# Performance work log

Measured on AMD Instinct MI355X. Metric: run time of the kernel, lower is better.

The kernel has to match this reference:

```python
import jax, jax.numpy as jnp
import numpy as np

N_NODES = 100000
N_EDGES = 1600000
NUM_FEATURES = 128
HIDDEN = 64
NUM_CLASSES = 2


def _gcn_norm(edge_index, num_nodes):
    # PyG gcn_norm: add self-loops, symmetric degree normalization.
    loop = jnp.arange(num_nodes, dtype=edge_index.dtype)
    src = jnp.concatenate([edge_index[0], loop])
    dst = jnp.concatenate([edge_index[1], loop])
    deg = jax.ops.segment_sum(jnp.ones_like(src, dtype=jnp.float32), dst,
                              num_segments=num_nodes)
    dinv = jnp.where(deg > 0, jax.lax.rsqrt(deg), 0.0)
    norm = dinv[src] * dinv[dst]  # [E + N]
    return src, dst, norm


def _gcn_conv(x, src, dst, norm, W, b, num_nodes):
    h = x @ W  # linear transform first (PyG GCNConv)
    msg = h[src] * norm[:, None]  # gather + edge scaling, [E+N, H]
    out = jax.ops.segment_sum(msg, dst, num_segments=num_nodes)  # scatter-add
    return out + b


def setup_inputs() -> dict:
    key = jax.random.key(0)
    ks = jax.random.split(key, 8)
    x = jax.random.normal(ks[0], (N_NODES, NUM_FEATURES), dtype=jnp.float32)
    edge_index = jax.random.randint(ks[1], (2, N_EDGES), 0, N_NODES, dtype=jnp.int32)
    def glorot(k, shape):
        lim = np.sqrt(6.0 / (shape[0] + shape[1]))
        return jax.random.uniform(k, shape, jnp.float32, -lim, lim)
    return {
        "x": x,
        "edge_index": edge_index,
        "W1": glorot(ks[2], (NUM_FEATURES, HIDDEN)),
        "b1": jnp.zeros((HIDDEN,), jnp.float32),
        "W2": glorot(ks[3], (HIDDEN, HIDDEN)),
        "b2": jnp.zeros((HIDDEN,), jnp.float32),
        "W3": glorot(ks[4], (HIDDEN, HIDDEN)),
        "b3": jnp.zeros((HIDDEN,), jnp.float32),
        "Wlin": glorot(ks[5], (HIDDEN, NUM_CLASSES)),
        "blin": jnp.zeros((NUM_CLASSES,), jnp.float32),
    }


def reference(x, edge_index, W1, b1, W2, b2, W3, b3, Wlin, blin):
    num_nodes = x.shape[0]
    src, dst, norm = _gcn_norm(edge_index, num_nodes)
    # eval mode: dropout is identity
    h = jax.nn.relu(_gcn_conv(x, src, dst, norm, W1, b1, num_nodes))
    h = jax.nn.relu(_gcn_conv(h, src, dst, norm, W2, b2, num_nodes))
    h = jax.nn.relu(_gcn_conv(h, src, dst, norm, W3, b3, num_nodes))
    logits = h @ Wlin + blin
    return jax.nn.log_softmax(logits, axis=1)
```

## Files before the change

kernel.cpp:

```cpp
#include <hip/hip_runtime.h>
#include <cstdint>
#include <cstddef>

#define NF 128
#define NH 64

typedef unsigned int uint32;

__device__ inline unsigned short f2bf(float f) {
  unsigned int u = __float_as_uint(f);
  return (unsigned short)((u + 0x7FFF + ((u >> 16) & 1)) >> 16);
}
__device__ inline float bf2f_lo(uint32 u) { return __uint_as_float(u << 16); }
__device__ inline float bf2f_hi(uint32 u) { return __uint_as_float(u & 0xFFFF0000u); }


__global__ __launch_bounds__(256) void count_kernel(const int* __restrict__ ei, int E,
                                                    int* __restrict__ cnt, int RW) {
  int pass = blockIdx.x & 7;
  int i = (blockIdx.x >> 3) * 256 + threadIdx.x;
  if (i * 4 >= E) return;
  int4 d = ((const int4*)(ei + E))[i];
  int lo = pass * RW, hi = lo + RW;
  if (d.x >= lo && d.x < hi) atomicAdd(&cnt[d.x], 1);
  if (d.y >= lo && d.y < hi) atomicAdd(&cnt[d.y], 1);
  if (d.z >= lo && d.z < hi) atomicAdd(&cnt[d.z], 1);
  if (d.w >= lo && d.w < hi) atomicAdd(&cnt[d.w], 1);
}

__global__ __launch_bounds__(256) void partial_kernel(const int* __restrict__ cnt, int N,
                                                      int* __restrict__ part) {
  __shared__ int sd[256];
  int t = threadIdx.x;
  int idx = blockIdx.x * 1024 + t * 4;
  int s = 0;
#pragma unroll
  for (int j = 0; j < 4; ++j)
    if (idx + j < N) s += cnt[idx + j];
  sd[t] = s;
  __syncthreads();
  for (int off = 128; off > 0; off >>= 1) {
    if (t < off) sd[t] += sd[t + off];
    __syncthreads();
  }
  if (t == 0) part[blockIdx.x] = sd[0];
}

__global__ __launch_bounds__(128) void scanp_kernel(int* __restrict__ part, int NB,
                                                    int* __restrict__ rowptrN) {
  __shared__ int s[128];
  int t = threadIdx.x;
  int v = (t < NB) ? part[t] : 0;
  s[t] = v;
  __syncthreads();
  for (int off = 1; off < 128; off <<= 1) {
    int add = (t >= off) ? s[t - off] : 0;
    __syncthreads();
    s[t] += add;
    __syncthreads();
  }
  if (t < NB) part[t] = s[t] - v;
  if (t == 0) rowptrN[0] = s[127];
}

__global__ __launch_bounds__(256) void rowptr_kernel(const int* __restrict__ cnt,
                                                     const int* __restrict__ part,
                                                     int* __restrict__ rowptr,
                                                     int* __restrict__ cnt2,
                                                     float* __restrict__ dinv, int N) {
  __shared__ int s[256];
  int t = threadIdx.x;
  int idx = blockIdx.x * 1024 + t * 4;
  int c[4];
  int ts = 0;
#pragma unroll
  for (int j = 0; j < 4; ++j) {
    c[j] = (idx + j < N) ? cnt[idx + j] : 0;
    ts += c[j];
  }
  s[t] = ts;
  __syncthreads();
  for (int off = 1; off < 256; off <<= 1) {
    int add = (t >= off) ? s[t - off] : 0;
    __syncthreads();
    s[t] += add;
    __syncthreads();
  }
  int run = s[t] - ts + part[blockIdx.x];
#pragma unroll
  for (int j = 0; j < 4; ++j) {
    if (idx + j < N) {
      rowptr[idx + j] = run;
      cnt2[idx + j] = run;
      dinv[idx + j] = rsqrtf((float)(c[j] + 1));
    }
    run += c[j];
  }
}

__global__ __launch_bounds__(256) void fill_kernel(const int* __restrict__ ei, int E,
                                                   int* __restrict__ cnt2,
                                                   const float* __restrict__ dinv,
                                                   int2* __restrict__ col2, int RW) {
  int pass = blockIdx.x & 7;
  int i = (blockIdx.x >> 3) * 256 + threadIdx.x;
  if (i * 4 >= E) return;
  int4 sv = ((const int4*)ei)[i];
  int4 dv = ((const int4*)(ei + E))[i];
  int lo = pass * RW, hi = lo + RW;
  int ss[4] = {sv.x, sv.y, sv.z, sv.w};
  int dd[4] = {dv.x, dv.y, dv.z, dv.w};
#pragma unroll
  for (int j = 0; j < 4; ++j) {
    int d = dd[j];
    if (d < lo || d >= hi) continue;
    int s = ss[j];
    float w = dinv[s] * dinv[d];
    int pos = atomicAdd(&cnt2[d], 1);
    col2[pos] = make_int2(s, __float_as_int(w));
  }
}


template <int K>
__global__ __launch_bounds__(256, 4) void gemm_kernel(const float* __restrict__ X,
                                                      const float* __restrict__ W,
                                                      uint32* __restrict__ Hb, int N) {
  __shared__ float XsT[64][68];
  __shared__ float Ws[64 * 64];
  const int tid = threadIdx.x;
  const int n0 = blockIdx.x * 64;
  const int tn = (tid >> 4) * 4;
  const int tf = (tid & 15) * 4;

  float acc[4][4];
#pragma unroll
  for (int i = 0; i < 4; ++i)
#pragma unroll
    for (int j = 0; j < 4; ++j) acc[i][j] = 0.f;

  for (int kt = 0; kt < K / 64; ++kt) {
    {
      const float4* Wg = (const float4*)(W + (size_t)kt * 64 * 64);
      float4* Wl = (float4*)Ws;
#pragma unroll
      for (int j = 0; j < 4; ++j) Wl[tid + j * 256] = Wg[tid + j * 256];
    }
#pragma unroll
    for (int j = 0; j < 4; ++j) {
      int idx = tid + j * 256;
      int n = idx >> 4;
      int kq = idx & 15;
      float4 v = make_float4(0.f, 0.f, 0.f, 0.f);
      if (n0 + n < N)
        v = *(const float4*)(X + (size_t)(n0 + n) * K + kt * 64 + kq * 4);
      XsT[kq * 4 + 0][n] = v.x;
      XsT[kq * 4 + 1][n] = v.y;
      XsT[kq * 4 + 2][n] = v.z;
      XsT[kq * 4 + 3][n] = v.w;
    }
    __syncthreads();
#pragma unroll 8
    for (int k = 0; k < 64; ++k) {
      float4 xv = *(const float4*)(&XsT[k][tn]);
      float4 wv = *(const float4*)(&Ws[k * 64 + tf]);
      acc[0][0] = fmaf(xv.x, wv.x, acc[0][0]);
      acc[0][1] = fmaf(xv.x, wv.y, acc[0][1]);
      acc[0][2] = fmaf(xv.x, wv.z, acc[0][2]);
      acc[0][3] = fmaf(xv.x, wv.w, acc[0][3]);
      acc[1][0] = fmaf(xv.y, wv.x, acc[1][0]);
      acc[1][1] = fmaf(xv.y, wv.y, acc[1][1]);
      acc[1][2] = fmaf(xv.y, wv.z, acc[1][2]);
      acc[1][3] = fmaf(xv.y, wv.w, acc[1][3]);
      acc[2][0] = fmaf(xv.z, wv.x, acc[2][0]);
      acc[2][1] = fmaf(xv.z, wv.y, acc[2][1]);
      acc[2][2] = fmaf(xv.z, wv.z, acc[2][2]);
      acc[2][3] = fmaf(xv.z, wv.w, acc[2][3]);
      acc[3][0] = fmaf(xv.w, wv.x, acc[3][0]);
      acc[3][1] = fmaf(xv.w, wv.y, acc[3][1]);
      acc[3][2] = fmaf(xv.w, wv.z, acc[3][2]);
      acc[3][3] = fmaf(xv.w, wv.w, acc[3][3]);
    }
    __syncthreads();
  }
#pragma unroll
  for (int i = 0; i < 4; ++i) {
    int n = n0 + tn + i;
    if (n < N) {
      uint32 p0 = (uint32)f2bf(acc[i][0]) | ((uint32)f2bf(acc[i][1]) << 16);
      uint32 p1 = (uint32)f2bf(acc[i][2]) | ((uint32)f2bf(acc[i][3]) << 16);
      *(uint2*)(Hb + (size_t)n * 32 + tf / 2) = make_uint2(p0, p1);
    }
  }
}

template <int FINAL>
__global__ __launch_bounds__(256) void prop_fused_kernel(
    const uint32* __restrict__ H32, const int* __restrict__ rowptr,
    const int2* __restrict__ col2, const float* __restrict__ dinv,
    const float* __restrict__ bias, const float* __restrict__ Wn,
    const float* __restrict__ blin, void* __restrict__ outv, int N) {
  __shared__ float Ws[64 * 64];
  __shared__ float rbuf[4][64];
  const int lane = threadIdx.x & 63;
  const int widx = threadIdx.x >> 6;
  const int fl = lane & 31;
  const int half = lane >> 5;

  if (!FINAL) {
    const float4* Wg = (const float4*)Wn;
    float4* Wl = (float4*)Ws;
    for (int i = threadIdx.x; i < 1024; i += 256) Wl[i] = Wg[i];
    __syncthreads();
  }

  int n = blockIdx.x * 4 + widx;
  n = __builtin_amdgcn_readfirstlane(n);
  if (n >= N) return;

  int e0 = rowptr[n];
  int e1 = rowptr[n + 1];
  float di = dinv[n];
  const int2* ec = col2 + e0;
  const int m = e1 - e0;

  float acc0 = 0.f, acc1 = 0.f;
  if (half == 0) {
    uint32 u = H32[(size_t)n * 32 + fl];
    float w = di * di;
    acc0 = bf2f_lo(u) * w;
    acc1 = bf2f_hi(u) * w;
  }

  const int npair = m >> 1;
  const int nfull = npair >> 3;
  for (int b = 0; b < nfull; ++b) {
    int s[8];
    float wv[8];
#pragma unroll
    for (int j = 0; j < 8; ++j) {
      int2 c = ec[2 * (b * 8 + j) + half];
      s[j] = c.x;
      wv[j] = __int_as_float(c.y);
    }
    uint32 u[8];
#pragma unroll
    for (int j = 0; j < 8; ++j) u[j] = H32[(size_t)s[j] * 32 + fl];
#pragma unroll
    for (int j = 0; j < 8; ++j) {
      acc0 = fmaf(wv[j], bf2f_lo(u[j]), acc0);
      acc1 = fmaf(wv[j], bf2f_hi(u[j]), acc1);
    }
  }
  for (int t = nfull * 8; t < npair; ++t) {
    int2 c = ec[2 * t + half];
    uint32 u = H32[(size_t)c.x * 32 + fl];
    float w = __int_as_float(c.y);
    acc0 = fmaf(w, bf2f_lo(u), acc0);
    acc1 = fmaf(w, bf2f_hi(u), acc1);
  }
  if ((m & 1) && half == 0) {
    int2 c = ec[m - 1];
    uint32 u = H32[(size_t)c.x * 32 + fl];
    float w = __int_as_float(c.y);
    acc0 = fmaf(w, bf2f_lo(u), acc0);
    acc1 = fmaf(w, bf2f_hi(u), acc1);
  }
  acc0 += __shfl_xor(acc0, 32, 64);
  acc1 += __shfl_xor(acc1, 32, 64);

  float2 bv = ((const float2*)bias)[fl];
  float r0 = acc0 + bv.x;
  float r1 = acc1 + bv.y;
  r0 = r0 > 0.f ? r0 : 0.f;
  r1 = r1 > 0.f ? r1 : 0.f;

  if (FINAL) {
    float t0 = 0.f, t1 = 0.f;
    if (half == 0) {
      t0 = r0 * Wn[4 * fl + 0] + r1 * Wn[4 * fl + 2];
      t1 = r0 * Wn[4 * fl + 1] + r1 * Wn[4 * fl + 3];
    }
#pragma unroll
    for (int off = 32; off > 0; off >>= 1) {
      t0 += __shfl_xor(t0, off, 64);
      t1 += __shfl_xor(t1, off, 64);
    }
    if (lane == 0) {
      float* out = (float*)outv;
      float l0 = t0 + blin[0];
      float l1 = t1 + blin[1];
      float mx = fmaxf(l0, l1);
      float lz = mx + logf(expf(l0 - mx) + expf(l1 - mx));
      out[(size_t)n * 2 + 0] = l0 - lz;
      out[(size_t)n * 2 + 1] = l1 - lz;
    }
  } else {
    if (half == 0) *(float2*)(&rbuf[widx][2 * fl]) = make_float2(r0, r1);
    __builtin_amdgcn_wave_barrier();
    float o = 0.f;
#pragma unroll
    for (int q = 0; q < 16; ++q) {
      float4 rv = *(const float4*)(&rbuf[widx][4 * q]);
      o = fmaf(rv.x, Ws[(4 * q + 0) * 64 + lane], o);
      o = fmaf(rv.y, Ws[(4 * q + 1) * 64 + lane], o);
      o = fmaf(rv.z, Ws[(4 * q + 2) * 64 + lane], o);
      o = fmaf(rv.w, Ws[(4 * q + 3) * 64 + lane], o);
    }
    ((unsigned short*)outv)[(size_t)n * 64 + lane] = f2bf(o);
  }
}


extern "C" void kernel_launch(void* const* d_in, const int* in_sizes, int n_in,
                              void* d_out, int out_size, void* d_ws, size_t ws_size,
                              hipStream_t stream) {
  const float* x  = (const float*)d_in[0];
  const int*   ei = (const int*)d_in[1];
  const float* W1 = (const float*)d_in[2];
  const float* b1 = (const float*)d_in[3];
  const float* W2 = (const float*)d_in[4];
  const float* b2 = (const float*)d_in[5];
  const float* W3 = (const float*)d_in[6];
  const float* b3 = (const float*)d_in[7];
  const float* Wl = (const float*)d_in[8];
  const float* bl = (const float*)d_in[9];
  float* out = (float*)d_out;

  const int N = in_sizes[0] / NF;
  const int E = in_sizes[1] / 2;

  char* w = (char*)d_ws;
  size_t off = 0;
  auto alloc = [&](size_t bytes) {
    void* p = w + off;
    off += bytes;
    off = (off + 15) & ~(size_t)15;
    return p;
  };
  int*    cnt    = (int*)alloc((size_t)N * 4);
  int*    cnt2   = (int*)alloc((size_t)N * 4);
  int*    rowptr = (int*)alloc((size_t)(N + 1) * 4);
  int*    part   = (int*)alloc(256 * 4);
  float*  dinv   = (float*)alloc((size_t)N * 4);
  int2*   col2   = (int2*)alloc((size_t)E * 8);
  uint32* hA     = (uint32*)alloc((size_t)N * 32 * 4);
  uint32* hB     = (uint32*)alloc((size_t)N * 32 * 4);

  const int NB = (N + 1023) / 1024;
  const int RW = (N + 7) / 8;
  const int NCHUNK = (E / 4 + 255) / 256;

  hipMemsetAsync(cnt, 0, (size_t)N * 4, stream);
  hipLaunchKernelGGL(count_kernel, dim3(8 * NCHUNK), dim3(256), 0, stream,
                     ei, E, cnt, RW);
  hipLaunchKernelGGL(partial_kernel, dim3(NB), dim3(256), 0, stream, cnt, N, part);
  hipLaunchKernelGGL(scanp_kernel, dim3(1), dim3(128), 0, stream, part, NB, rowptr + N);
  hipLaunchKernelGGL(rowptr_kernel, dim3(NB), dim3(256), 0, stream,
                     cnt, part, rowptr, cnt2, dinv, N);
  hipLaunchKernelGGL(fill_kernel, dim3(8 * NCHUNK), dim3(256), 0, stream,
                     ei, E, cnt2, dinv, col2, RW);

  hipLaunchKernelGGL(gemm_kernel<128>, dim3((N + 63) / 64), dim3(256), 0, stream,
                     x, W1, hA, N);
  hipLaunchKernelGGL(prop_fused_kernel<0>, dim3((N + 3) / 4), dim3(256), 0, stream,
                     hA, rowptr, col2, dinv, b1, W2, (const float*)nullptr, (void*)hB, N);
  hipLaunchKernelGGL(prop_fused_kernel<0>, dim3((N + 3) / 4), dim3(256), 0, stream,
                     hB, rowptr, col2, dinv, b2, W3, (const float*)nullptr, (void*)hA, N);
  hipLaunchKernelGGL(prop_fused_kernel<1>, dim3((N + 3) / 4), dim3(256), 0, stream,
                     hA, rowptr, col2, dinv, b3, Wl, bl, (void*)out, N);
}
```

Before: 444.9 us.

## Use bf16 MFMA for first GEMM, halve CSR build passes, shrink final LDS

Replaces the fp32 LDS-tiled first-layer GEMM with a bf16 MFMA 16x16x32 kernel that loads X and W directly from global memory and converts them to bf16 in registers. The count and fill kernels for CSR construction now partition destinations into 4 ranges instead of 8, cutting redundant reads of the edge index at the cost of a wider atomic range per pass. The final propagation kernel's shared-memory allocation shrinks because it does not use the weight tile. Rounding inputs to bf16 before the GEMM adds precision loss, and the scalar 2-byte output stores are not coalesced.

```diff
diff --git a/kernel.cpp b/kernel.cpp
--- a/kernel.cpp
+++ b/kernel.cpp
@@ -6,6 +6,8 @@
 #define NH 64
 
 typedef unsigned int uint32;
+typedef short bf16x8 __attribute__((ext_vector_type(8)));
+typedef float f32x4 __attribute__((ext_vector_type(4)));
 
 __device__ inline unsigned short f2bf(float f) {
   unsigned int u = __float_as_uint(f);
@@ -17,8 +19,8 @@
 
 __global__ __launch_bounds__(256) void count_kernel(const int* __restrict__ ei, int E,
                                                     int* __restrict__ cnt, int RW) {
-  int pass = blockIdx.x & 7;
-  int i = (blockIdx.x >> 3) * 256 + threadIdx.x;
+  int pass = blockIdx.x & 3;
+  int i = (blockIdx.x >> 2) * 256 + threadIdx.x;
   if (i * 4 >= E) return;
   int4 d = ((const int4*)(ei + E))[i];
   int lo = pass * RW, hi = lo + RW;
@@ -102,8 +104,8 @@
                                                    int* __restrict__ cnt2,
                                                    const float* __restrict__ dinv,
                                                    int2* __restrict__ col2, int RW) {
-  int pass = blockIdx.x & 7;
-  int i = (blockIdx.x >> 3) * 256 + threadIdx.x;
+  int pass = blockIdx.x & 3;
+  int i = (blockIdx.x >> 2) * 256 + threadIdx.x;
   if (i * 4 >= E) return;
   int4 sv = ((const int4*)ei)[i];
   int4 dv = ((const int4*)(ei + E))[i];
@@ -122,77 +124,53 @@
 }
 
 
-template <int K>
-__global__ __launch_bounds__(256, 4) void gemm_kernel(const float* __restrict__ X,
-                                                      const float* __restrict__ W,
-                                                      uint32* __restrict__ Hb, int N) {
-  __shared__ float XsT[64][68];
-  __shared__ float Ws[64 * 64];
-  const int tid = threadIdx.x;
-  const int n0 = blockIdx.x * 64;
-  const int tn = (tid >> 4) * 4;
-  const int tf = (tid & 15) * 4;
-
-  float acc[4][4];
-#pragma unroll
-  for (int i = 0; i < 4; ++i)
-#pragma unroll
-    for (int j = 0; j < 4; ++j) acc[i][j] = 0.f;
-
-  for (int kt = 0; kt < K / 64; ++kt) {
-    {
-      const float4* Wg = (const float4*)(W + (size_t)kt * 64 * 64);
-      float4* Wl = (float4*)Ws;
-#pragma unroll
-      for (int j = 0; j < 4; ++j) Wl[tid + j * 256] = Wg[tid + j * 256];
-    }
-#pragma unroll
-    for (int j = 0; j < 4; ++j) {
-      int idx = tid + j * 256;
-      int n = idx >> 4;
-      int kq = idx & 15;
-      float4 v = make_float4(0.f, 0.f, 0.f, 0.f);
-      if (n0 + n < N)
-        v = *(const float4*)(X + (size_t)(n0 + n) * K + kt * 64 + kq * 4);
-      XsT[kq * 4 + 0][n] = v.x;
-      XsT[kq * 4 + 1][n] = v.y;
-      XsT[kq * 4 + 2][n] = v.z;
-      XsT[kq * 4 + 3][n] = v.w;
-    }
-    __syncthreads();
-#pragma unroll 8
-    for (int k = 0; k < 64; ++k) {
-      float4 xv = *(const float4*)(&XsT[k][tn]);
-      float4 wv = *(const float4*)(&Ws[k * 64 + tf]);
-      acc[0][0] = fmaf(xv.x, wv.x, acc[0][0]);
-      acc[0][1] = fmaf(xv.x, wv.y, acc[0][1]);
-      acc[0][2] = fmaf(xv.x, wv.z, acc[0][2]);
-      acc[0][3] = fmaf(xv.x, wv.w, acc[0][3]);
-      acc[1][0] = fmaf(xv.y, wv.x, acc[1][0]);
-      acc[1][1] = fmaf(xv.y, wv.y, acc[1][1]);
-      acc[1][2] = fmaf(xv.y, wv.z, acc[1][2]);
-      acc[1][3] = fmaf(xv.y, wv.w, acc[1][3]);
-      acc[2][0] = fmaf(xv.z, wv.x, acc[2][0]);
-      acc[2][1] = fmaf(xv.z, wv.y, acc[2][1]);
-      acc[2][2] = fmaf(xv.z, wv.z, acc[2][2]);
-      acc[2][3] = fmaf(xv.z, wv.w, acc[2][3]);
-      acc[3][0] = fmaf(xv.w, wv.x, acc[3][0]);
-      acc[3][1] = fmaf(xv.w, wv.y, acc[3][1]);
-      acc[3][2] = fmaf(xv.w, wv.z, acc[3][2]);
-      acc[3][3] = fmaf(xv.w, wv.w, acc[3][3]);
-    }
-    __syncthreads();
-  }
-#pragma unroll
-  for (int i = 0; i < 4; ++i) {
-    int n = n0 + tn + i;
+__global__ __launch_bounds__(256) void gemm1_mfma_kernel(
+    const float* __restrict__ X, const float* __restrict__ W,
+    uint32* __restrict__ Hb, int N) {
+  const int lane = threadIdx.x & 63;
+  const int wv = threadIdx.x >> 6;
+  const int m = lane & 15;
+  const int g = lane >> 4;
+  const int base = blockIdx.x * 64 + wv * 16;
+  int row = base + m;
+  int rowc = row < N ? row : N - 1;
+  const float* xp = X + (size_t)rowc * 128 + g * 8;
+
+  f32x4 acc[4];
+#pragma unroll
+  for (int nt = 0; nt < 4; ++nt) acc[nt] = (f32x4){0.f, 0.f, 0.f, 0.f};
+
+#pragma unroll
+  for (int kk = 0; kk < 4; ++kk) {
+    float4 alo = *(const float4*)(xp + kk * 32);
+    float4 ahi = *(const float4*)(xp + kk * 32 + 4);
+    bf16x8 a;
+    a[0] = (short)f2bf(alo.x); a[1] = (short)f2bf(alo.y);
+    a[2] = (short)f2bf(alo.z); a[3] = (short)f2bf(alo.w);
+    a[4] = (short)f2bf(ahi.x); a[5] = (short)f2bf(ahi.y);
+    a[6] = (short)f2bf(ahi.z); a[7] = (short)f2bf(ahi.w);
+    const float* wp = W + (size_t)(kk * 32 + g * 8) * 64 + m;
+#pragma unroll
+    for (int nt = 0; nt < 4; ++nt) {
+      bf16x8 b;
+#pragma unroll
+      for (int i = 0; i < 8; ++i)
+        b[i] = (short)f2bf(wp[(size_t)i * 64 + nt * 16]);
+      acc[nt] = __builtin_amdgcn_mfma_f32_16x16x32_bf16(a, b, acc[nt], 0, 0, 0);
+    }
+  }
+  unsigned short* Hs = (unsigned short*)Hb;
+#pragma unroll
+  for (int j = 0; j < 4; ++j) {
+    int n = base + g * 4 + j;
     if (n < N) {
-      uint32 p0 = (uint32)f2bf(acc[i][0]) | ((uint32)f2bf(acc[i][1]) << 16);
-      uint32 p1 = (uint32)f2bf(acc[i][2]) | ((uint32)f2bf(acc[i][3]) << 16);
-      *(uint2*)(Hb + (size_t)n * 32 + tf / 2) = make_uint2(p0, p1);
-    }
-  }
-}
+#pragma unroll
+      for (int nt = 0; nt < 4; ++nt)
+        Hs[(size_t)n * 64 + nt * 16 + m] = f2bf(acc[nt][j]);
+    }
+  }
+}
+
 
 template <int FINAL>
 __global__ __launch_bounds__(256) void prop_fused_kernel(
@@ -200,8 +178,8 @@
     const int2* __restrict__ col2, const float* __restrict__ dinv,
     const float* __restrict__ bias, const float* __restrict__ Wn,
     const float* __restrict__ blin, void* __restrict__ outv, int N) {
-  __shared__ float Ws[64 * 64];
-  __shared__ float rbuf[4][64];
+  __shared__ float Ws[FINAL ? 4 : 64 * 64];
+  __shared__ float rbuf[FINAL ? 1 : 4][64];
   const int lane = threadIdx.x & 63;
   const int widx = threadIdx.x >> 6;
   const int fl = lane & 31;
@@ -348,20 +326,20 @@
   uint32* hB     = (uint32*)alloc((size_t)N * 32 * 4);
 
   const int NB = (N + 1023) / 1024;
-  const int RW = (N + 7) / 8;
+  const int RW4 = (N + 3) / 4;
   const int NCHUNK = (E / 4 + 255) / 256;
 
   hipMemsetAsync(cnt, 0, (size_t)N * 4, stream);
-  hipLaunchKernelGGL(count_kernel, dim3(8 * NCHUNK), dim3(256), 0, stream,
-                     ei, E, cnt, RW);
+  hipLaunchKernelGGL(count_kernel, dim3(4 * NCHUNK), dim3(256), 0, stream,
+                     ei, E, cnt, RW4);
   hipLaunchKernelGGL(partial_kernel, dim3(NB), dim3(256), 0, stream, cnt, N, part);
   hipLaunchKernelGGL(scanp_kernel, dim3(1), dim3(128), 0, stream, part, NB, rowptr + N);
   hipLaunchKernelGGL(rowptr_kernel, dim3(NB), dim3(256), 0, stream,
                      cnt, part, rowptr, cnt2, dinv, N);
-  hipLaunchKernelGGL(fill_kernel, dim3(8 * NCHUNK), dim3(256), 0, stream,
-                     ei, E, cnt2, dinv, col2, RW);
-
-  hipLaunchKernelGGL(gemm_kernel<128>, dim3((N + 63) / 64), dim3(256), 0, stream,
+  hipLaunchKernelGGL(fill_kernel, dim3(4 * NCHUNK), dim3(256), 0, stream,
+                     ei, E, cnt2, dinv, col2, RW4);
+
+  hipLaunchKernelGGL(gemm1_mfma_kernel, dim3((N + 63) / 64), dim3(256), 0, stream,
                      x, W1, hA, N);
   hipLaunchKernelGGL(prop_fused_kernel<0>, dim3((N + 3) / 4), dim3(256), 0, stream,
                      hA, rowptr, col2, dinv, b1, W2, (const float*)nullptr, (void*)hB, N);
```

Measured after the change: 428.7 us. -3.6%, faster.
